# Kernel tuning notes

Hardware: AMD Instinct MI355X
Metric: run time of the kernel (lower is better)

## Reference

```python
import jax, jax.numpy as jnp
import numpy as np

# Module constants (from init_kwargs)
NOISE_NUM = 64
SAMPLE_NUM = 262144
FCL = 65                 # filter_coeff_length
FL = 64                  # frame_length
GAIN = 1.0               # attenuate_gain
FRAME_NUM = SAMPLE_NUM // FL + 1   # 4097
IR = 2 * FCL - 1         # 129, linear-phase IR length
CONV = IR + FL - 1       # 192, per-frame filtered length
LOG10 = float(np.log(10.0))


def modified_sigmoid(x):
    # DDSP modified sigmoid: 2*sigmoid(x)^log(10) + 1e-7
    return 2.0 * jax.nn.sigmoid(x) ** LOG10 + 1e-7


def setup_inputs() -> dict:
    key = jax.random.key(0)
    k1, k2 = jax.random.split(key)
    coefficient_bank = jax.random.uniform(k1, (NOISE_NUM, FRAME_NUM, FCL),
                                          dtype=jnp.float32, minval=-1.0, maxval=1.0)
    noise = jax.random.uniform(k2, (NOISE_NUM, FRAME_NUM, FL), dtype=jnp.float32)
    return {"coefficient_bank": coefficient_bank, "noise": noise}


def reference(coefficient_bank, noise):
    B, F, L = coefficient_bank.shape  # (64, 4097, 65)
    # Zero-phase frequency response -> impulse response
    fr = modified_sigmoid(coefficient_bank)                  # (B,F,L) real half-spectrum
    zp_ir = jnp.fft.irfft(fr, n=IR, axis=-1)                 # (B,F,129)
    lp_ir = jnp.roll(zp_ir, L - 1, axis=-1)                  # linear phase
    # periodic hann window of length IR (torch.hann_window periodic=True)
    win = 0.5 * (1.0 - jnp.cos(2.0 * jnp.pi * jnp.arange(IR, dtype=jnp.float32) / IR))
    wir = lp_ir * win
    # FFT-domain filtering of per-frame noise (linear convolution length CONV)
    H = jnp.fft.rfft(jnp.pad(wir, ((0, 0), (0, 0), (0, FL - 1))), axis=-1)   # (B,F,97)
    n = noise * 2.0 - 1.0                                                    # uniform [-1,1)
    N = jnp.fft.rfft(jnp.pad(n, ((0, 0), (0, 0), (0, IR - 1))), axis=-1)     # (B,F,97)
    filtered = jnp.fft.irfft(N * H, n=CONV, axis=-1) * GAIN                  # (B,F,192)
    # Overlap-add with hop FL (replaces conv_transpose1d with identity kernel)
    total = (F - 1) * FL + CONV
    idx = (jnp.arange(F)[:, None] * FL + jnp.arange(CONV)[None, :]).reshape(-1)
    out = jnp.zeros((B, total), dtype=filtered.dtype).at[:, idx].add(filtered.reshape(B, -1))
    return out[:, :SAMPLE_NUM]
```

## Files before the change

### kernel.cpp

```cpp
#include <hip/hip_runtime.h>


#define NB 64
#define FTOT 4097
#define FCL 65
#define FL 64
#define SAMPLES 262144
#define OUT_FRAMES 4096
#define G 16
#define NF (G + 2)
#define NSTRIDE 68
#define PW 260
#define BLOCKS_PER_B (OUT_FRAMES / G)

__device__ __forceinline__ float mod_sigmoid(float x) {
    float s = 1.0f / (1.0f + __expf(-x));
    return 2.0f * __expf(2.302585092994046f * __logf(s)) + 1e-7f;
}

__device__ __forceinline__ float rdlane(float v, int k) {
    return __int_as_float(__builtin_amdgcn_readlane(__float_as_int(v), k));
}

__global__ __launch_bounds__(128) void fn_kernel(
    const float* __restrict__ coeff,
    const float* __restrict__ noise,
    float* __restrict__ out)
{
    __shared__ __align__(16) float costab[132];
    __shared__ __align__(16) float nS[NF * NSTRIDE];
    __shared__ __align__(16) float wirP[NF * PW];

    const int tid  = threadIdx.x;
    const int lane = tid & 63;
    const int wv   = tid >> 6;
    const int blk  = blockIdx.x;
    const int b    = blk / BLOCKS_PER_B;
    const int cg   = blk % BLOCKS_PER_B;
    const int fp0  = cg * G;
    const int fbase = fp0 - 2;

    for (int i = tid; i < NF * PW / 4; i += 128)
        ((float4*)wirP)[i] = make_float4(0.f, 0.f, 0.f, 0.f);
    for (int i = tid; i < 129; i += 128)
        costab[i] = __cosf(6.283185307179586f * (float)i * (1.0f / 129.0f));

    for (int i = tid; i < NF * 16; i += 128) {
        int q = i >> 4, g = i & 15;
        int f = fbase + q;
        float4 v = make_float4(0.f, 0.f, 0.f, 0.f);
        if (f >= 0) {
            const float4* src = (const float4*)(noise + ((size_t)b * FTOT + f) * FL);
            float4 u = src[g];
            v = make_float4(2.f*u.x-1.f, 2.f*u.y-1.f, 2.f*u.z-1.f, 2.f*u.w-1.f);
        }
        *(float4*)&nS[q * NSTRIDE + 4 * g] = v;
    }

    float frv[9], f64v[9];
    #pragma unroll
    for (int i = 0; i < 9; ++i) {
        int f = fbase + wv + 2 * i;
        if (f < 0) f = 0;
        const float* row = coeff + ((size_t)b * FTOT + f) * FCL;
        frv[i]  = row[lane];
        f64v[i] = row[64];
    }
    #pragma unroll
    for (int i = 0; i < 9; ++i) {
        frv[i]  = mod_sigmoid(frv[i]);
        f64v[i] = mod_sigmoid(f64v[i]);
    }

    __syncthreads();

    {
        float c  = costab[lane];
        float c2 = 2.0f * c;
        float cp = 1.0f;
        float ck = c;
        float S[9];
        #pragma unroll
        for (int i = 0; i < 9; ++i) S[i] = 0.5f * rdlane(frv[i], 0);
        #pragma unroll 8
        for (int k = 1; k < 64; ++k) {
            #pragma unroll
            for (int i = 0; i < 9; ++i)
                S[i] = __builtin_fmaf(rdlane(frv[i], k), ck, S[i]);
            float cn = __builtin_fmaf(c2, ck, -cp);
            cp = ck; ck = cn;
        }
        #pragma unroll
        for (int i = 0; i < 9; ++i)
            S[i] = __builtin_fmaf(f64v[i], ck, S[i]);
        float w1f = 0.5f - 0.5f * costab[64 + lane];
        float w2f = 0.5f - 0.5f * costab[64 - lane];
        #pragma unroll
        for (int i = 0; i < 9; ++i) {
            int fi = wv + 2 * i;
            float zp = S[i] * (2.0f / 129.0f);
            wirP[fi * PW + 127 + lane] = w1f * zp;
            wirP[fi * PW + 127 - lane] = w2f * zp;
        }
    }
    __syncthreads();

    {
        const int chunk = tid >> 3;
        const int r0    = (tid & 7) * 8;
        float a[8];
        #pragma unroll
        for (int j = 0; j < 8; ++j) a[j] = 0.0f;

        #pragma unroll
        for (int dd = 0; dd < 3; ++dd) {
            const int q = chunk + 2 - dd;
            const float* wb = &wirP[q * PW + 63 + 64 * dd + r0];
            const float4* n4p = (const float4*)&nS[q * NSTRIDE];
            float4 W1 = *(const float4*)(wb + 1);
            float4 W2 = *(const float4*)(wb + 5);
            #pragma unroll
            for (int s4 = 0; s4 < 16; ++s4) {
                float4 W0 = *(const float4*)(wb - 3 - 4 * s4);
                float4 n4 = n4p[s4];
                float w[11] = {W0.x, W0.y, W0.z, W0.w,
                               W1.x, W1.y, W1.z, W1.w,
                               W2.x, W2.y, W2.z};
                float nv[4] = {n4.x, n4.y, n4.z, n4.w};
                #pragma unroll
                for (int i = 0; i < 4; ++i)
                    #pragma unroll
                    for (int j = 0; j < 8; ++j)
                        a[j] = __builtin_fmaf(nv[i], w[j - i + 3], a[j]);
                W2 = W1; W1 = W0;
            }
        }

        float* op = &out[(size_t)b * SAMPLES + (size_t)fp0 * 64 + (size_t)tid * 8];
        *(float4*)op       = make_float4(a[0], a[1], a[2], a[3]);
        *(float4*)(op + 4) = make_float4(a[4], a[5], a[6], a[7]);
    }
}

extern "C" void kernel_launch(void* const* d_in, const int* in_sizes, int n_in,
                              void* d_out, int out_size, void* d_ws, size_t ws_size,
                              hipStream_t stream) {
    const float* coeff = (const float*)d_in[0];
    const float* noise = (const float*)d_in[1];
    float* out = (float*)d_out;
    dim3 grid(NB * BLOCKS_PER_B);
    fn_kernel<<<grid, 128, 0, stream>>>(coeff, noise, out);
}
```

Before: 293.6 us.

## Skip zero-padded convolution terms and remap threads to frame chunks

The convolution phase now skips multiply-adds against the zero-padded parts of the windowed impulse response. Threads are remapped so each wave handles one half of the output offsets, and the first and last delay terms iterate only over the half of noise samples that overlap nonzero IR taps. The padded IR buffer stride shrinks, which cuts LDS use, and launch bounds now request 4 blocks per CU. The result is different wave branches (wave-uniform) and a changed LDS access pattern, which may cause bank conflicts with the new stride.

Result: faster. 278.8 us (-5.0%).

```diff
diff --git a/kernel.cpp b/kernel.cpp
--- a/kernel.cpp
+++ b/kernel.cpp
@@ -4,13 +4,12 @@
 #define NB 64
 #define FTOT 4097
 #define FCL 65
-#define FL 64
 #define SAMPLES 262144
 #define OUT_FRAMES 4096
 #define G 16
 #define NF (G + 2)
 #define NSTRIDE 68
-#define PW 260
+#define PW 196
 #define BLOCKS_PER_B (OUT_FRAMES / G)
 
 __device__ __forceinline__ float mod_sigmoid(float x) {
@@ -22,7 +21,30 @@
     return __int_as_float(__builtin_amdgcn_readlane(__float_as_int(v), k));
 }
 
-__global__ __launch_bounds__(128) void fn_kernel(
+template<int S0, int S1>
+__device__ __forceinline__ void conv_dd(const float4* __restrict__ wq,
+                                        const float4* __restrict__ nq,
+                                        float a[8]) {
+    float4 W1 = wq[-S0];
+    float4 W2 = wq[-S0 + 1];
+    #pragma unroll
+    for (int s4 = S0; s4 < S1; ++s4) {
+        float4 W0 = wq[-s4 - 1];
+        float4 n4 = nq[s4];
+        float w[12] = {W0.x, W0.y, W0.z, W0.w,
+                       W1.x, W1.y, W1.z, W1.w,
+                       W2.x, W2.y, W2.z, W2.w};
+        float nv[4] = {n4.x, n4.y, n4.z, n4.w};
+        #pragma unroll
+        for (int i = 0; i < 4; ++i)
+            #pragma unroll
+            for (int j = 0; j < 8; ++j)
+                a[j] = __builtin_fmaf(nv[i], w[4 + j - i], a[j]);
+        W2 = W1; W1 = W0;
+    }
+}
+
+__global__ __launch_bounds__(128, 4) void fn_kernel(
     const float* __restrict__ coeff,
     const float* __restrict__ noise,
     float* __restrict__ out)
@@ -50,7 +72,7 @@
         int f = fbase + q;
         float4 v = make_float4(0.f, 0.f, 0.f, 0.f);
         if (f >= 0) {
-            const float4* src = (const float4*)(noise + ((size_t)b * FTOT + f) * FL);
+            const float4* src = (const float4*)(noise + ((size_t)b * FTOT + f) * 64);
             float4 u = src[g];
             v = make_float4(2.f*u.x-1.f, 2.f*u.y-1.f, 2.f*u.z-1.f, 2.f*u.w-1.f);
         }
@@ -99,44 +121,41 @@
         for (int i = 0; i < 9; ++i) {
             int fi = wv + 2 * i;
             float zp = S[i] * (2.0f / 129.0f);
-            wirP[fi * PW + 127 + lane] = w1f * zp;
-            wirP[fi * PW + 127 - lane] = w2f * zp;
+            wirP[fi * PW + 96 + lane] = w1f * zp;
+            wirP[fi * PW + 96 - lane] = w2f * zp;
         }
     }
     __syncthreads();
 
     {
-        const int chunk = tid >> 3;
-        const int r0    = (tid & 7) * 8;
+        const int chunk = tid & 15;
+        const int t     = tid >> 4;
         float a[8];
         #pragma unroll
         for (int j = 0; j < 8; ++j) a[j] = 0.0f;
 
-        #pragma unroll
-        for (int dd = 0; dd < 3; ++dd) {
-            const int q = chunk + 2 - dd;
-            const float* wb = &wirP[q * PW + 63 + 64 * dd + r0];
-            const float4* n4p = (const float4*)&nS[q * NSTRIDE];
-            float4 W1 = *(const float4*)(wb + 1);
-            float4 W2 = *(const float4*)(wb + 5);
-            #pragma unroll
-            for (int s4 = 0; s4 < 16; ++s4) {
-                float4 W0 = *(const float4*)(wb - 3 - 4 * s4);
-                float4 n4 = n4p[s4];
-                float w[11] = {W0.x, W0.y, W0.z, W0.w,
-                               W1.x, W1.y, W1.z, W1.w,
-                               W2.x, W2.y, W2.z};
-                float nv[4] = {n4.x, n4.y, n4.z, n4.w};
-                #pragma unroll
-                for (int i = 0; i < 4; ++i)
-                    #pragma unroll
-                    for (int j = 0; j < 8; ++j)
-                        a[j] = __builtin_fmaf(nv[i], w[j - i + 3], a[j]);
-                W2 = W1; W1 = W0;
-            }
+        {
+            const int q = chunk + 2;
+            const float4* wq = (const float4*)&wirP[q * PW] + (8 + 2 * t);
+            const float4* nq = (const float4*)&nS[q * NSTRIDE];
+            if (wv == 0) conv_dd<0, 8>(wq, nq, a);
+            else         conv_dd<0, 16>(wq, nq, a);
+        }
+        {
+            const int q = chunk + 1;
+            const float4* wq = (const float4*)&wirP[q * PW] + (24 + 2 * t);
+            const float4* nq = (const float4*)&nS[q * NSTRIDE];
+            conv_dd<0, 16>(wq, nq, a);
+        }
+        {
+            const int q = chunk;
+            const float4* wq = (const float4*)&wirP[q * PW] + (40 + 2 * t);
+            const float4* nq = (const float4*)&nS[q * NSTRIDE];
+            if (wv == 0) conv_dd<0, 16>(wq, nq, a);
+            else         conv_dd<8, 16>(wq, nq, a);
         }
 
-        float* op = &out[(size_t)b * SAMPLES + (size_t)fp0 * 64 + (size_t)tid * 8];
+        float* op = &out[(size_t)b * SAMPLES + (size_t)(fp0 + chunk) * 64 + t * 8];
         *(float4*)op       = make_float4(a[0], a[1], a[2], a[3]);
         *(float4*)(op + 4) = make_float4(a[4], a[5], a[6], a[7]);
     }
```

## Double frames per block, skip zero-weight taps, read noise directly from global

Applied to the files above, without the earlier changes.

Each block now covers 32 output frames with 256 threads instead of 16 frames with 128, so the two halo frames whose impulse responses are recomputed are spread over more useful output. The convolution loop bounds now skip the parts of the 129-tap window that are known zeros, which cuts FMAs, and the shared wirP row stride shrinks to match. Noise is no longer staged in LDS; it is read from global memory as float4 and scaled inside the inner loop, and the cosine table is replaced by per-lane __cosf calls. This lowers LDS traffic and setup cost but adds repeated global loads and per-thread trig, and changes occupancy through launch_bounds(256,5).

Result: slower. 301.1 us (+2.6%).

```diff
diff --git a/kernel.cpp b/kernel.cpp
--- a/kernel.cpp
+++ b/kernel.cpp
@@ -4,13 +4,11 @@
 #define NB 64
 #define FTOT 4097
 #define FCL 65
-#define FL 64
 #define SAMPLES 262144
 #define OUT_FRAMES 4096
-#define G 16
+#define G 32
 #define NF (G + 2)
-#define NSTRIDE 68
-#define PW 260
+#define PW 196
 #define BLOCKS_PER_B (OUT_FRAMES / G)
 
 __device__ __forceinline__ float mod_sigmoid(float x) {
@@ -22,13 +20,36 @@
     return __int_as_float(__builtin_amdgcn_readlane(__float_as_int(v), k));
 }
 
-__global__ __launch_bounds__(128) void fn_kernel(
+__device__ __forceinline__ void conv_dd(const float4* __restrict__ wb,
+                                        const float4* __restrict__ np4,
+                                        int S0, int S1, float a[8]) {
+    float4 W1 = wb[16 - S0];
+    float4 W2 = wb[17 - S0];
+    #pragma unroll 4
+    for (int s4 = S0; s4 < S1; ++s4) {
+        float4 W0 = wb[15 - s4];
+        float4 u  = np4[s4];
+        float nv[4] = {__builtin_fmaf(u.x, 2.f, -1.f),
+                       __builtin_fmaf(u.y, 2.f, -1.f),
+                       __builtin_fmaf(u.z, 2.f, -1.f),
+                       __builtin_fmaf(u.w, 2.f, -1.f)};
+        float w[12] = {W0.x, W0.y, W0.z, W0.w,
+                       W1.x, W1.y, W1.z, W1.w,
+                       W2.x, W2.y, W2.z, W2.w};
+        #pragma unroll
+        for (int i = 0; i < 4; ++i)
+            #pragma unroll
+            for (int j = 0; j < 8; ++j)
+                a[j] = __builtin_fmaf(nv[i], w[4 + j - i], a[j]);
+        W2 = W1; W1 = W0;
+    }
+}
+
+__global__ __launch_bounds__(256, 5) void fn_kernel(
     const float* __restrict__ coeff,
     const float* __restrict__ noise,
     float* __restrict__ out)
 {
-    __shared__ __align__(16) float costab[132];
-    __shared__ __align__(16) float nS[NF * NSTRIDE];
     __shared__ __align__(16) float wirP[NF * PW];
 
     const int tid  = threadIdx.x;
@@ -40,29 +61,20 @@
     const int fp0  = cg * G;
     const int fbase = fp0 - 2;
 
-    for (int i = tid; i < NF * PW / 4; i += 128)
-        ((float4*)wirP)[i] = make_float4(0.f, 0.f, 0.f, 0.f);
-    for (int i = tid; i < 129; i += 128)
-        costab[i] = __cosf(6.283185307179586f * (float)i * (1.0f / 129.0f));
-
-    for (int i = tid; i < NF * 16; i += 128) {
-        int q = i >> 4, g = i & 15;
-        int f = fbase + q;
-        float4 v = make_float4(0.f, 0.f, 0.f, 0.f);
-        if (f >= 0) {
-            const float4* src = (const float4*)(noise + ((size_t)b * FTOT + f) * FL);
-            float4 u = src[g];
-            v = make_float4(2.f*u.x-1.f, 2.f*u.y-1.f, 2.f*u.z-1.f, 2.f*u.w-1.f);
-        }
-        *(float4*)&nS[q * NSTRIDE + 4 * g] = v;
+    for (int i = tid; i < NF * 18; i += 256) {
+        int row = i / 18, z = i - row * 18;
+        int qz = (z < 9) ? z : (z + 31);
+        ((float4*)wirP)[row * 49 + qz] = make_float4(0.f, 0.f, 0.f, 0.f);
     }
 
-    float frv[9], f64v[9];
+    float frv[9], f64v[9], vm[9];
     #pragma unroll
     for (int i = 0; i < 9; ++i) {
-        int f = fbase + wv + 2 * i;
-        if (f < 0) f = 0;
-        const float* row = coeff + ((size_t)b * FTOT + f) * FCL;
+        int fi = wv + 4 * i;
+        int f  = fbase + fi;
+        vm[i] = (f >= 0 && fi < NF) ? 1.f : 0.f;
+        int fl = f < 0 ? 0 : (f > FTOT - 1 ? FTOT - 1 : f);
+        const float* row = coeff + ((size_t)b * FTOT + fl) * FCL;
         frv[i]  = row[lane];
         f64v[i] = row[64];
     }
@@ -75,7 +87,7 @@
     __syncthreads();
 
     {
-        float c  = costab[lane];
+        float c  = __cosf(6.283185307179586f * (float)lane * (1.0f / 129.0f));
         float c2 = 2.0f * c;
         float cp = 1.0f;
         float ck = c;
@@ -93,50 +105,40 @@
         #pragma unroll
         for (int i = 0; i < 9; ++i)
             S[i] = __builtin_fmaf(f64v[i], ck, S[i]);
-        float w1f = 0.5f - 0.5f * costab[64 + lane];
-        float w2f = 0.5f - 0.5f * costab[64 - lane];
+        float w1f = 0.5f - 0.5f * __cosf(6.283185307179586f * (float)(64 + lane) * (1.0f / 129.0f));
+        float w2f = 0.5f - 0.5f * __cosf(6.283185307179586f * (float)(64 - lane) * (1.0f / 129.0f));
         #pragma unroll
         for (int i = 0; i < 9; ++i) {
-            int fi = wv + 2 * i;
-            float zp = S[i] * (2.0f / 129.0f);
-            wirP[fi * PW + 127 + lane] = w1f * zp;
-            wirP[fi * PW + 127 - lane] = w2f * zp;
+            int fi = wv + 4 * i;
+            if (fi < NF) {
+                float zp = S[i] * (2.0f / 129.0f) * vm[i];
+                wirP[fi * PW + 96 + lane] = w1f * zp;
+                wirP[fi * PW + 96 - lane] = w2f * zp;
+            }
         }
     }
     __syncthreads();
 
     {
-        const int chunk = tid >> 3;
-        const int r0    = (tid & 7) * 8;
+        const int chunk = tid & 31;
+        const int t     = tid >> 5;
         float a[8];
         #pragma unroll
         for (int j = 0; j < 8; ++j) a[j] = 0.0f;
 
         #pragma unroll
         for (int dd = 0; dd < 3; ++dd) {
-            const int q = chunk + 2 - dd;
-            const float* wb = &wirP[q * PW + 63 + 64 * dd + r0];
-            const float4* n4p = (const float4*)&nS[q * NSTRIDE];
-            float4 W1 = *(const float4*)(wb + 1);
-            float4 W2 = *(const float4*)(wb + 5);
-            #pragma unroll
-            for (int s4 = 0; s4 < 16; ++s4) {
-                float4 W0 = *(const float4*)(wb - 3 - 4 * s4);
-                float4 n4 = n4p[s4];
-                float w[11] = {W0.x, W0.y, W0.z, W0.w,
-                               W1.x, W1.y, W1.z, W1.w,
-                               W2.x, W2.y, W2.z};
-                float nv[4] = {n4.x, n4.y, n4.z, n4.w};
-                #pragma unroll
-                for (int i = 0; i < 4; ++i)
-                    #pragma unroll
-                    for (int j = 0; j < 8; ++j)
-                        a[j] = __builtin_fmaf(nv[i], w[j - i + 3], a[j]);
-                W2 = W1; W1 = W0;
-            }
+            const int q  = chunk + 2 - dd;
+            const int fq = fbase + q;
+            const int fc = fq < 0 ? 0 : fq;
+            const float4* np4 = (const float4*)(noise + ((size_t)b * FTOT + fc) * 64);
+            const float4* wb  = (const float4*)wirP + q * 49 + (16 * dd + 2 * t - 8);
+            int S0 = (dd == 2) ? 4 * wv : 0;
+            int S1 = (dd == 0) ? 4 * wv + 4 : 16;
+            conv_dd(wb, np4, S0, S1, a);
         }
 
-        float* op = &out[(size_t)b * SAMPLES + (size_t)fp0 * 64 + (size_t)tid * 8];
+        float* op = &out[(size_t)b * SAMPLES + (size_t)(fp0 + chunk) * 64 + t * 8];
         *(float4*)op       = make_float4(a[0], a[1], a[2], a[3]);
         *(float4*)(op + 4) = make_float4(a[4], a[5], a[6], a[7]);
     }
@@ -149,5 +151,5 @@
     const float* noise = (const float*)d_in[1];
     float* out = (float*)d_out;
     dim3 grid(NB * BLOCKS_PER_B);
-    fn_kernel<<<grid, 128, 0, stream>>>(coeff, noise, out);
+    fn_kernel<<<grid, 256, 0, stream>>>(coeff, noise, out);
 }
```
